# Kernel optimization log

Measured on AMD Instinct MI355X. Metric: run time of the kernel, lower is better.

## Reference

```python
import jax, jax.numpy as jnp
import numpy as np

N_STEPS = 2
MAX_STEP = 1.0
EPS64 = float(np.finfo(np.float64).eps)


def _sphere_log(p, q):
    # log map on unit sphere, tangent at p pointing to q; p,q: [..., D]
    cos = jnp.clip(jnp.sum(p * q, axis=-1, keepdims=True), -1.0, 1.0)
    u = q - cos * p
    un = jnp.linalg.norm(u, axis=-1, keepdims=True)
    theta = jnp.arccos(cos)
    return theta * u / (un + 1e-12)


def _sphere_exp(p, v):
    # exp map on unit sphere; jnp.sinc(n/pi) = sin(n)/n (stable at 0)
    n = jnp.linalg.norm(v, axis=-1, keepdims=True)
    x = jnp.cos(n) * p + jnp.sinc(n / jnp.pi) * v
    return x / jnp.linalg.norm(x, axis=-1, keepdims=True)


def setup_inputs() -> dict:
    key = jax.random.key(0)
    ks = jax.random.split(key, 6)
    N, C, D, E = 50000, 16, 3, 1600000
    nodes = jax.random.normal(ks[0], (N, C, D), dtype=jnp.float32)
    nodes = nodes / jnp.linalg.norm(nodes, axis=-1, keepdims=True)  # points on S^2
    edge_w = jax.random.uniform(ks[1], (E,), dtype=jnp.float32)
    senders = jax.random.randint(ks[2], (E,), 0, N, dtype=jnp.int32)
    receivers = jax.random.randint(ks[3], (E,), 0, N, dtype=jnp.int32)
    t_sqrt = 1.0 + 0.3 * jax.random.normal(ks[4], (C,), dtype=jnp.float32)
    delta_sqrt = 1.0 + 0.3 * jax.random.normal(ks[5], (C,), dtype=jnp.float32)
    return {"nodes": nodes, "edge_w": edge_w, "t_sqrt": t_sqrt,
            "delta_sqrt": delta_sqrt, "senders": senders, "receivers": receivers}


def reference(nodes, edge_w, t_sqrt, delta_sqrt, senders, receivers):
    N = nodes.shape[0]
    t = (t_sqrt ** 2) / N_STEPS            # per-channel time, split across Euler steps
    delta = delta_sqrt ** 2                 # per-channel min step size
    deg = jax.ops.segment_sum(edge_w, senders, num_segments=N)  # [N]

    def laplace(x):
        # graph Laplacian of manifold-valued signal: weighted mean of log maps, negated
        logs = _sphere_log(x[senders], x[receivers])              # [E, C, D]
        agg = jax.ops.segment_sum(edge_w[:, None, None] * logs, senders, num_segments=N)
        return -agg / (deg[:, None, None] + 1e-12)                # [N, C, D]

    def step(x, _):
        v = laplace(x)
        nrm = jnp.sqrt(jnp.sum(v * v, axis=-1) + EPS64)           # [N, C]
        alp = jax.nn.sigmoid(nrm - delta[None, :])
        scale = jnp.where(nrm * alp <= MAX_STEP, alp, MAX_STEP / nrm)
        v = -(v * scale[..., None]) * t[None, :, None]
        return _sphere_exp(x, v), None

    x, _ = jax.lax.scan(step, nodes, None, length=N_STEPS, unroll=N_STEPS)
    return x
```

## Files before the change

kernel.cpp:

```cpp
#include <hip/hip_runtime.h>
#include <math.h>


constexpr float EPS64F = 2.2204460492503131e-16f;
constexpr float PI_F   = 3.14159265358979323846f;
constexpr int   NREP   = 8;

typedef int   vi4 __attribute__((ext_vector_type(4)));
typedef float vf4 __attribute__((ext_vector_type(4)));
typedef float vf2 __attribute__((ext_vector_type(2)));


__global__ __launch_bounds__(256) void hist_kernel(
    const vi4* __restrict__ snd4, int* __restrict__ rep,
    vi4* __restrict__ pos4, const int* __restrict__ snd,
    int* __restrict__ pos, int N, int E) {
  int tid = threadIdx.x;
  int E4 = E >> 2;
  #pragma unroll
  for (int gg = 0; gg < 4; ++gg) {
    int g = blockIdx.x * 1024 + gg * 256 + tid;
    if (g < E4) {
      int rb = (g & (NREP - 1)) * N;
      vi4 s = __builtin_nontemporal_load(&snd4[g]);
      vi4 p;
      p.x = atomicAdd(&rep[rb + s.x], 1);
      p.y = atomicAdd(&rep[rb + s.y], 1);
      p.z = atomicAdd(&rep[rb + s.z], 1);
      p.w = atomicAdd(&rep[rb + s.w], 1);
      __builtin_nontemporal_store(p, &pos4[g]);
    }
  }
  if (blockIdx.x == 0 && tid == 0) {
    for (int e = E4 << 2; e < E; ++e) pos[e] = atomicAdd(&rep[snd[e]], 1);
  }
}

__global__ __launch_bounds__(1024) void scanA_kernel(
    int* __restrict__ rep, int* __restrict__ row_start,
    int* __restrict__ btot, int N) {
  __shared__ int wsum[16];
  int tid = threadIdx.x;
  int lane = tid & 63, wave = tid >> 6;
  int i = blockIdx.x * 1024 + tid;
  int v = 0;
  if (i < N) {
    int run = 0;
    int cpre[NREP];
    #pragma unroll
    for (int r = 0; r < NREP; ++r) {
      int t = rep[r * N + i];
      cpre[r] = run;
      run += t;
    }
    v = run;
    #pragma unroll
    for (int r = 0; r < NREP; ++r) rep[r * N + i] = cpre[r];
  }
  int incl = v;
  #pragma unroll
  for (int off = 1; off < 64; off <<= 1) {
    int t = __shfl_up(incl, off, 64);
    if (lane >= off) incl += t;
  }
  if (lane == 63) wsum[wave] = incl;
  __syncthreads();
  if (wave == 0 && lane < 16) {
    int wincl = wsum[lane];
    #pragma unroll
    for (int off = 1; off < 16; off <<= 1) {
      int t = __shfl_up(wincl, off, 64);
      if (lane >= off) wincl += t;
    }
    wsum[lane] = wincl;
  }
  __syncthreads();
  int woff = (wave > 0) ? wsum[wave - 1] : 0;
  if (i < N) row_start[i] = woff + incl - v;
  if (tid == 0) btot[blockIdx.x] = wsum[15];
}

__global__ __launch_bounds__(64) void scanB_kernel(
    const int* __restrict__ btot, int* __restrict__ boff,
    int* __restrict__ row_start, int nb, int N) {
  int lane = threadIdx.x;
  int v = (lane < nb) ? btot[lane] : 0;
  int incl = v;
  #pragma unroll
  for (int off = 1; off < 64; off <<= 1) {
    int t = __shfl_up(incl, off, 64);
    if (lane >= off) incl += t;
  }
  if (lane < nb) boff[lane] = incl - v;
  if (lane == 63) row_start[N] = incl;
}

__global__ __launch_bounds__(1024) void scanC_kernel(
    int* __restrict__ row_start, const int* __restrict__ boff,
    int* __restrict__ rep, int N) {
  int i = blockIdx.x * 1024 + threadIdx.x;
  if (i < N) {
    int rs = row_start[i] + boff[blockIdx.x];
    row_start[i] = rs;
    #pragma unroll
    for (int r = 0; r < NREP; ++r) rep[r * N + i] += rs;
  }
}

__global__ __launch_bounds__(256) void fill_kernel(
    const vi4* __restrict__ snd4, const vi4* __restrict__ rcv4,
    const vf4* __restrict__ ew4, const vi4* __restrict__ pos4,
    const int* __restrict__ rep, long long* __restrict__ pair,
    const int* __restrict__ snd, const int* __restrict__ rcv,
    const float* __restrict__ ew, const int* __restrict__ pos, int N, int E) {
  int tid = threadIdx.x;
  int E4 = E >> 2;
  #pragma unroll
  for (int gg = 0; gg < 2; ++gg) {
    int g = blockIdx.x * 512 + gg * 256 + tid;
    if (g < E4) {
      int rb = (g & (NREP - 1)) * N;
      vi4 s = __builtin_nontemporal_load(&snd4[g]);
      vi4 r = __builtin_nontemporal_load(&rcv4[g]);
      vf4 w = __builtin_nontemporal_load(&ew4[g]);
      vi4 p = __builtin_nontemporal_load(&pos4[g]);
      pair[rep[rb + s.x] + p.x] =
          (long long)(((unsigned long long)(unsigned)__float_as_int(w.x) << 32) | (unsigned)(r.x * 48));
      pair[rep[rb + s.y] + p.y] =
          (long long)(((unsigned long long)(unsigned)__float_as_int(w.y) << 32) | (unsigned)(r.y * 48));
      pair[rep[rb + s.z] + p.z] =
          (long long)(((unsigned long long)(unsigned)__float_as_int(w.z) << 32) | (unsigned)(r.z * 48));
      pair[rep[rb + s.w] + p.w] =
          (long long)(((unsigned long long)(unsigned)__float_as_int(w.w) << 32) | (unsigned)(r.w * 48));
    }
  }
  if (blockIdx.x == 0 && tid == 0) {
    for (int e = E4 << 2; e < E; ++e) {
      pair[rep[snd[e]] + pos[e]] =
          (long long)(((unsigned long long)(unsigned)__float_as_int(ew[e]) << 32) | (unsigned)(rcv[e] * 48));
    }
    for (int z = 0; z < 16; ++z) pair[(size_t)E + z] = 0;
  }
}


__device__ __forceinline__ void edge_accum_pk(
    vf2 p0, vf2 p1, vf2 p2, vf2 q0, vf2 q1, vf2 q2, vf2 w,
    vf2& a0, vf2& a1, vf2& a2) {
  vf2 cs = p0 * q0 + p1 * q1 + p2 * q2;
  cs = __builtin_elementwise_min(vf2{1.f, 1.f},
       __builtin_elementwise_max(vf2{-1.f, -1.f}, cs));
  vf2 u0 = q0 - cs * p0;
  vf2 u1 = q1 - cs * p1;
  vf2 u2 = q2 - cs * p2;
  vf2 un2 = __builtin_elementwise_max(u0 * u0 + u1 * u1 + u2 * u2,
                                      vf2{1e-24f, 1e-24f});
  vf2 ax = __builtin_elementwise_abs(cs);
  vf2 s = __builtin_elementwise_sqrt(vf2{1.f, 1.f} - ax);
  vf2 poly = ((ax * -0.0187293f + 0.0742610f) * ax - 0.2121144f) * ax
             + 1.5707288f;
  vf2 th = s * poly;
  vf2 theta;
  theta.x = (cs.x >= 0.0f) ? th.x : (PI_F - th.x);
  theta.y = (cs.y >= 0.0f) ? th.y : (PI_F - th.y);
  vf2 rsq;
  rsq.x = __builtin_amdgcn_rsqf(un2.x);
  rsq.y = __builtin_amdgcn_rsqf(un2.y);
  vf2 coef = w * theta * rsq;
  a0 += coef * u0;
  a1 += coef * u1;
  a2 += coef * u2;
}

__device__ __forceinline__ void node_step(
    float a0, float a1, float a2, float ws, float p0, float p1, float p2,
    float ts, float dsv, float& y0, float& y1, float& y2) {
  float invdg = __builtin_amdgcn_rcpf(ws + 1e-12f);
  float g0 = a0 * invdg, g1 = a1 * invdg, g2 = a2 * invdg;
  float nrm = sqrtf(fmaf(g0, g0, fmaf(g1, g1, g2 * g2)) + EPS64F);
  float tch = ts * ts * 0.5f;
  float dch = dsv * dsv;
  float alp = __builtin_amdgcn_rcpf(1.0f + __expf(dch - nrm));
  float scale = (nrm * alp <= 1.0f) ? alp : __builtin_amdgcn_rcpf(nrm);
  float f = scale * tch;
  float v0 = g0 * f, v1 = g1 * f, v2 = g2 * f;
  float nv = sqrtf(fmaf(v0, v0, fmaf(v1, v1, v2 * v2)));
  float cn = __cosf(nv);
  float sc = (nv > 1e-20f) ? (__sinf(nv) * __builtin_amdgcn_rcpf(nv)) : 1.0f;
  float t0 = fmaf(cn, p0, sc * v0);
  float t1 = fmaf(cn, p1, sc * v1);
  float t2 = fmaf(cn, p2, sc * v2);
  float inv = __builtin_amdgcn_rsqf(fmaf(t0, t0, fmaf(t1, t1, t2 * t2)));
  y0 = t0 * inv; y1 = t1 * inv; y2 = t2 * inv;
}

__global__ __launch_bounds__(256) void flowp_kernel(
    const float* __restrict__ xin, const int* __restrict__ row_start,
    const long long* __restrict__ pair, const float* __restrict__ tsq,
    const float* __restrict__ dsq, float* __restrict__ xout, int N) {
  int node = blockIdx.x * 4 + (threadIdx.x >> 6);
  if (node >= N) return;
  int lane = threadIdx.x & 63;
  int c = lane & 15;
  int k = lane >> 4;
  int c3 = c * 3;
  int beg = row_start[node];
  int end = row_start[node + 1];
  int ip = node * 48 + c3;
  float ps0 = xin[ip], ps1 = xin[ip + 1], ps2 = xin[ip + 2];
  vf2 p0 = {ps0, ps0}, p1 = {ps1, ps1}, p2 = {ps2, ps2};
  vf2 a0 = {0.f, 0.f}, a1 = {0.f, 0.f}, a2 = {0.f, 0.f}, wsv = {0.f, 0.f};
  int iters = (end - beg + 15) >> 4;
  int j = beg + k;
  for (int t = 0; t < iters; ++t, j += 16) {
    long long e0 = __builtin_nontemporal_load(&pair[j]);
    long long e1 = __builtin_nontemporal_load(&pair[j + 4]);
    long long e2 = __builtin_nontemporal_load(&pair[j + 8]);
    long long e3 = __builtin_nontemporal_load(&pair[j + 12]);
    float w0 = (j      < end) ? __int_as_float((int)(e0 >> 32)) : 0.f;
    float w1 = (j + 4  < end) ? __int_as_float((int)(e1 >> 32)) : 0.f;
    float w2 = (j + 8  < end) ? __int_as_float((int)(e2 >> 32)) : 0.f;
    float w3 = (j + 12 < end) ? __int_as_float((int)(e3 >> 32)) : 0.f;
    const float* q0p = xin + ((int)e0 + c3);
    const float* q1p = xin + ((int)e1 + c3);
    const float* q2p = xin + ((int)e2 + c3);
    const float* q3p = xin + ((int)e3 + c3);
    float qa0 = q0p[0], qa1 = q0p[1], qa2 = q0p[2];
    float qb0 = q1p[0], qb1 = q1p[1], qb2 = q1p[2];
    float qc0 = q2p[0], qc1 = q2p[1], qc2 = q2p[2];
    float qd0 = q3p[0], qd1 = q3p[1], qd2 = q3p[2];
    vf2 wA = {w0, w1}, wB = {w2, w3};
    edge_accum_pk(p0, p1, p2, vf2{qa0, qb0}, vf2{qa1, qb1}, vf2{qa2, qb2},
                  wA, a0, a1, a2);
    edge_accum_pk(p0, p1, p2, vf2{qc0, qd0}, vf2{qc1, qd1}, vf2{qc2, qd2},
                  wB, a0, a1, a2);
    wsv += wA + wB;
  }
  float A0 = a0.x + a0.y, A1 = a1.x + a1.y, A2 = a2.x + a2.y;
  float ws = wsv.x + wsv.y;
  A0 += __shfl_xor(A0, 16); A1 += __shfl_xor(A1, 16);
  A2 += __shfl_xor(A2, 16); ws += __shfl_xor(ws, 16);
  A0 += __shfl_xor(A0, 32); A1 += __shfl_xor(A1, 32);
  A2 += __shfl_xor(A2, 32); ws += __shfl_xor(ws, 32);
  if (k == 0) {
    float y0, y1, y2;
    node_step(A0, A1, A2, ws, ps0, ps1, ps2, tsq[c], dsq[c], y0, y1, y2);
    xout[ip] = y0; xout[ip + 1] = y1; xout[ip + 2] = y2;
  }
}

static inline size_t al16(size_t x) { return (x + 15) & ~(size_t)15; }

extern "C" void kernel_launch(void* const* d_in, const int* in_sizes, int n_in,
                              void* d_out, int out_size, void* d_ws, size_t ws_size,
                              hipStream_t stream) {
  const float* nodes = (const float*)d_in[0];
  const float* ew    = (const float*)d_in[1];
  const float* tsq   = (const float*)d_in[2];
  const float* dsq   = (const float*)d_in[3];
  const int*   snd   = (const int*)d_in[4];
  const int*   rcv   = (const int*)d_in[5];
  float* out = (float*)d_out;

  int E = in_sizes[1];
  int N = in_sizes[0] / 48;

  size_t repB  = al16((size_t)NREP * N * 4);
  size_t rsB   = al16((size_t)(N + 4) * 4);
  size_t auxB  = 512;
  size_t pairB = al16((size_t)(E + 16) * 8);

  char* base = (char*)d_ws;
  int*       rep       = (int*)base;
  int*       row_start = (int*)(base + repB);
  int*       btot      = (int*)(base + repB + rsB);
  int*       boff      = btot + 64;
  long long* pair      = (long long*)(base + repB + rsB + auxB);
  char*      after     = base + repB + rsB + auxB + pairB;
  int*       pos       = (int*)after;
  float*     xtmp      = (float*)after;

  hipMemsetAsync(rep, 0, repB, stream);

  int E4 = E >> 2;
  int hb  = (E4 + 1023) / 1024;
  int fbk = (E4 + 511) / 512;
  int nb  = (N + 1023) / 1024;
  int nfb = (N + 3) / 4;

  hist_kernel<<<hb, 256, 0, stream>>>((const vi4*)snd, rep, (vi4*)pos,
                                      snd, pos, N, E);
  scanA_kernel<<<nb, 1024, 0, stream>>>(rep, row_start, btot, N);
  scanB_kernel<<<1, 64, 0, stream>>>(btot, boff, row_start, nb, N);
  scanC_kernel<<<nb, 1024, 0, stream>>>(row_start, boff, rep, N);
  fill_kernel<<<fbk, 256, 0, stream>>>((const vi4*)snd, (const vi4*)rcv,
                                       (const vf4*)ew, (const vi4*)pos,
                                       rep, pair, snd, rcv, ew, pos, N, E);

  flowp_kernel<<<nfb, 256, 0, stream>>>(nodes, row_start, pair, tsq, dsq, xtmp, N);
  flowp_kernel<<<nfb, 256, 0, stream>>>(xtmp, row_start, pair, tsq, dsq, out, N);
}
```

Baseline: 309.1 us.

## Pad node coordinates to float4 for single vector gathers in flow kernels

Converts the node array from packed xyz (12 bytes per channel) to a padded float4 layout, so each neighbor gather in the edge loop becomes one 16-byte load instead of three scalar loads. The pair index now encodes receiver*16 in float4 units, and the intermediate state between the two steps is kept padded. A fallback path handles small workspaces by gathering from the original layout in the first step. This adds a conversion kernel and a third more gathered bytes per node, and sets a launch-bounds occupancy hint.

Measured after the change: 340.7 us. 1.1x slower.

```diff
diff --git a/kernel.cpp b/kernel.cpp
--- a/kernel.cpp
+++ b/kernel.cpp
@@ -125,22 +125,32 @@
       vf4 w = __builtin_nontemporal_load(&ew4[g]);
       vi4 p = __builtin_nontemporal_load(&pos4[g]);
       pair[rep[rb + s.x] + p.x] =
-          (long long)(((unsigned long long)(unsigned)__float_as_int(w.x) << 32) | (unsigned)(r.x * 48));
+          (long long)(((unsigned long long)(unsigned)__float_as_int(w.x) << 32) | (unsigned)(r.x * 16));
       pair[rep[rb + s.y] + p.y] =
-          (long long)(((unsigned long long)(unsigned)__float_as_int(w.y) << 32) | (unsigned)(r.y * 48));
+          (long long)(((unsigned long long)(unsigned)__float_as_int(w.y) << 32) | (unsigned)(r.y * 16));
       pair[rep[rb + s.z] + p.z] =
-          (long long)(((unsigned long long)(unsigned)__float_as_int(w.z) << 32) | (unsigned)(r.z * 48));
+          (long long)(((unsigned long long)(unsigned)__float_as_int(w.z) << 32) | (unsigned)(r.z * 16));
       pair[rep[rb + s.w] + p.w] =
-          (long long)(((unsigned long long)(unsigned)__float_as_int(w.w) << 32) | (unsigned)(r.w * 48));
+          (long long)(((unsigned long long)(unsigned)__float_as_int(w.w) << 32) | (unsigned)(r.w * 16));
     }
   }
   if (blockIdx.x == 0 && tid == 0) {
     for (int e = E4 << 2; e < E; ++e) {
       pair[rep[snd[e]] + pos[e]] =
-          (long long)(((unsigned long long)(unsigned)__float_as_int(ew[e]) << 32) | (unsigned)(rcv[e] * 48));
+          (long long)(((unsigned long long)(unsigned)__float_as_int(ew[e]) << 32) | (unsigned)(rcv[e] * 16));
     }
     for (int z = 0; z < 16; ++z) pair[(size_t)E + z] = 0;
   }
+}
+
+
+__global__ __launch_bounds__(256) void conv_kernel(
+    const float* __restrict__ xf, vf4* __restrict__ xp, int NC) {
+  int t = blockIdx.x * 256 + threadIdx.x;
+  if (t >= NC) return;
+  vf4 v;
+  v.x = xf[t * 3]; v.y = xf[t * 3 + 1]; v.z = xf[t * 3 + 2]; v.w = 0.f;
+  xp[t] = v;
 }
 
 
@@ -194,10 +204,66 @@
   y0 = t0 * inv; y1 = t1 * inv; y2 = t2 * inv;
 }
 
-__global__ __launch_bounds__(256) void flowp_kernel(
-    const float* __restrict__ xin, const int* __restrict__ row_start,
+__global__ __launch_bounds__(256, 8) void flow4_kernel(
+    const vf4* __restrict__ xp, const int* __restrict__ row_start,
     const long long* __restrict__ pair, const float* __restrict__ tsq,
-    const float* __restrict__ dsq, float* __restrict__ xout, int N) {
+    const float* __restrict__ dsq, vf4* __restrict__ yp,
+    float* __restrict__ out48, int N) {
+  int node = blockIdx.x * 4 + (threadIdx.x >> 6);
+  if (node >= N) return;
+  int lane = threadIdx.x & 63;
+  int c = lane & 15;
+  int k = lane >> 4;
+  int beg = row_start[node];
+  int end = row_start[node + 1];
+  vf4 p = xp[node * 16 + c];
+  vf2 p0 = {p.x, p.x}, p1 = {p.y, p.y}, p2 = {p.z, p.z};
+  vf2 a0 = {0.f, 0.f}, a1 = {0.f, 0.f}, a2 = {0.f, 0.f}, wsv = {0.f, 0.f};
+  int iters = (end - beg + 15) >> 4;
+  int j = beg + k;
+  for (int t = 0; t < iters; ++t, j += 16) {
+    long long e0 = __builtin_nontemporal_load(&pair[j]);
+    long long e1 = __builtin_nontemporal_load(&pair[j + 4]);
+    long long e2 = __builtin_nontemporal_load(&pair[j + 8]);
+    long long e3 = __builtin_nontemporal_load(&pair[j + 12]);
+    float w0 = (j      < end) ? __int_as_float((int)(e0 >> 32)) : 0.f;
+    float w1 = (j + 4  < end) ? __int_as_float((int)(e1 >> 32)) : 0.f;
+    float w2 = (j + 8  < end) ? __int_as_float((int)(e2 >> 32)) : 0.f;
+    float w3 = (j + 12 < end) ? __int_as_float((int)(e3 >> 32)) : 0.f;
+    vf4 qa = xp[(int)e0 + c];
+    vf4 qb = xp[(int)e1 + c];
+    vf4 qc = xp[(int)e2 + c];
+    vf4 qd = xp[(int)e3 + c];
+    vf2 wA = {w0, w1}, wB = {w2, w3};
+    edge_accum_pk(p0, p1, p2, vf2{qa.x, qb.x}, vf2{qa.y, qb.y},
+                  vf2{qa.z, qb.z}, wA, a0, a1, a2);
+    edge_accum_pk(p0, p1, p2, vf2{qc.x, qd.x}, vf2{qc.y, qd.y},
+                  vf2{qc.z, qd.z}, wB, a0, a1, a2);
+    wsv += wA + wB;
+  }
+  float A0 = a0.x + a0.y, A1 = a1.x + a1.y, A2 = a2.x + a2.y;
+  float ws = wsv.x + wsv.y;
+  A0 += __shfl_xor(A0, 16); A1 += __shfl_xor(A1, 16);
+  A2 += __shfl_xor(A2, 16); ws += __shfl_xor(ws, 16);
+  A0 += __shfl_xor(A0, 32); A1 += __shfl_xor(A1, 32);
+  A2 += __shfl_xor(A2, 32); ws += __shfl_xor(ws, 32);
+  if (k == 0) {
+    float y0, y1, y2;
+    node_step(A0, A1, A2, ws, p.x, p.y, p.z, tsq[c], dsq[c], y0, y1, y2);
+    if (out48) {
+      int ip = node * 48 + c * 3;
+      out48[ip] = y0; out48[ip + 1] = y1; out48[ip + 2] = y2;
+    } else {
+      vf4 v; v.x = y0; v.y = y1; v.z = y2; v.w = 0.f;
+      yp[node * 16 + c] = v;
+    }
+  }
+}
+
+__global__ __launch_bounds__(256) void flow3_kernel(
+    const float* __restrict__ x48, const int* __restrict__ row_start,
+    const long long* __restrict__ pair, const float* __restrict__ tsq,
+    const float* __restrict__ dsq, vf4* __restrict__ yp, int N) {
   int node = blockIdx.x * 4 + (threadIdx.x >> 6);
   if (node >= N) return;
   int lane = threadIdx.x & 63;
@@ -207,7 +273,7 @@
   int beg = row_start[node];
   int end = row_start[node + 1];
   int ip = node * 48 + c3;
-  float ps0 = xin[ip], ps1 = xin[ip + 1], ps2 = xin[ip + 2];
+  float ps0 = x48[ip], ps1 = x48[ip + 1], ps2 = x48[ip + 2];
   vf2 p0 = {ps0, ps0}, p1 = {ps1, ps1}, p2 = {ps2, ps2};
   vf2 a0 = {0.f, 0.f}, a1 = {0.f, 0.f}, a2 = {0.f, 0.f}, wsv = {0.f, 0.f};
   int iters = (end - beg + 15) >> 4;
@@ -221,10 +287,10 @@
     float w1 = (j + 4  < end) ? __int_as_float((int)(e1 >> 32)) : 0.f;
     float w2 = (j + 8  < end) ? __int_as_float((int)(e2 >> 32)) : 0.f;
     float w3 = (j + 12 < end) ? __int_as_float((int)(e3 >> 32)) : 0.f;
-    const float* q0p = xin + ((int)e0 + c3);
-    const float* q1p = xin + ((int)e1 + c3);
-    const float* q2p = xin + ((int)e2 + c3);
-    const float* q3p = xin + ((int)e3 + c3);
+    const float* q0p = x48 + ((int)e0 * 3 + c3);
+    const float* q1p = x48 + ((int)e1 * 3 + c3);
+    const float* q2p = x48 + ((int)e2 * 3 + c3);
+    const float* q3p = x48 + ((int)e3 * 3 + c3);
     float qa0 = q0p[0], qa1 = q0p[1], qa2 = q0p[2];
     float qb0 = q1p[0], qb1 = q1p[1], qb2 = q1p[2];
     float qc0 = q2p[0], qc1 = q2p[1], qc2 = q2p[2];
@@ -245,7 +311,8 @@
   if (k == 0) {
     float y0, y1, y2;
     node_step(A0, A1, A2, ws, ps0, ps1, ps2, tsq[c], dsq[c], y0, y1, y2);
-    xout[ip] = y0; xout[ip + 1] = y1; xout[ip + 2] = y2;
+    vf4 v; v.x = y0; v.y = y1; v.z = y2; v.w = 0.f;
+    yp[node * 16 + c] = v;
   }
 }
 
@@ -269,6 +336,10 @@
   size_t rsB   = al16((size_t)(N + 4) * 4);
   size_t auxB  = 512;
   size_t pairB = al16((size_t)(E + 16) * 8);
+  size_t xpB   = al16((size_t)N * 16 * 16);
+  size_t posB  = al16((size_t)E * 4);
+  size_t zB    = (posB > xpB) ? posB : xpB;
+  size_t need_main = repB + rsB + auxB + pairB + xpB + zB;
 
   char* base = (char*)d_ws;
   int*       rep       = (int*)base;
@@ -277,8 +348,12 @@
   int*       boff      = btot + 64;
   long long* pair      = (long long*)(base + repB + rsB + auxB);
   char*      after     = base + repB + rsB + auxB + pairB;
-  int*       pos       = (int*)after;
-  float*     xtmp      = (float*)after;
+
+  bool mainp = (ws_size >= need_main);
+  vf4* xpA = (vf4*)after;
+  char* zreg = mainp ? (after + xpB) : after;
+  int* pos = (int*)zreg;
+  vf4* xpB_ = (vf4*)zreg;
 
   hipMemsetAsync(rep, 0, repB, stream);
 
@@ -286,8 +361,10 @@
   int hb  = (E4 + 1023) / 1024;
   int fbk = (E4 + 511) / 512;
   int nb  = (N + 1023) / 1024;
+  int cb  = (N * 16 + 255) / 256;
   int nfb = (N + 3) / 4;
 
+  if (mainp) conv_kernel<<<cb, 256, 0, stream>>>(nodes, xpA, N * 16);
   hist_kernel<<<hb, 256, 0, stream>>>((const vi4*)snd, rep, (vi4*)pos,
                                       snd, pos, N, E);
   scanA_kernel<<<nb, 1024, 0, stream>>>(rep, row_start, btot, N);
@@ -297,6 +374,15 @@
                                        (const vf4*)ew, (const vi4*)pos,
                                        rep, pair, snd, rcv, ew, pos, N, E);
 
-  flowp_kernel<<<nfb, 256, 0, stream>>>(nodes, row_start, pair, tsq, dsq, xtmp, N);
-  flowp_kernel<<<nfb, 256, 0, stream>>>(xtmp, row_start, pair, tsq, dsq, out, N);
-}
+  if (mainp) {
+    flow4_kernel<<<nfb, 256, 0, stream>>>(xpA, row_start, pair, tsq, dsq,
+                                          xpB_, (float*)0, N);
+    flow4_kernel<<<nfb, 256, 0, stream>>>(xpB_, row_start, pair, tsq, dsq,
+                                          (vf4*)0, out, N);
+  } else {
+    flow3_kernel<<<nfb, 256, 0, stream>>>(nodes, row_start, pair, tsq, dsq,
+                                          xpB_, N);
+    flow4_kernel<<<nfb, 256, 0, stream>>>(xpB_, row_start, pair, tsq, dsq,
+                                          (vf4*)0, out, N);
+  }
+}
```

## Replace global-atomic sender histogram with chunked LDS histograms and byte offsets

Applied to the files above, without the earlier changes.

Builds the CSR for the edge list with per-chunk shared-memory histograms instead of global atomics on replicated counters. Edges are split into 32K-edge chunks and sender ranges of 16K nodes, and the within-bucket positions are stored as bytes. A per-chunk scan then produces base offsets for the fill kernel. This removes global atomic contention and the memset, and shrinks the position array. In exchange every chunk block rereads the sender array once per sender range, there are extra scan passes over a chunk-by-N offset table, and the byte positions assume fewer than 256 edges per sender in each chunk.

Result: faster. 298.4 us (-3.4%).

```diff
diff --git a/kernel.cpp b/kernel.cpp
--- a/kernel.cpp
+++ b/kernel.cpp
@@ -4,59 +4,71 @@
 
 constexpr float EPS64F = 2.2204460492503131e-16f;
 constexpr float PI_F   = 3.14159265358979323846f;
-constexpr int   NREP   = 8;
+constexpr int   SR_BITS = 14;
+constexpr int   CH_BITS = 15;
 
 typedef int   vi4 __attribute__((ext_vector_type(4)));
 typedef float vf4 __attribute__((ext_vector_type(4)));
 typedef float vf2 __attribute__((ext_vector_type(2)));
 
 
-__global__ __launch_bounds__(256) void hist_kernel(
-    const vi4* __restrict__ snd4, int* __restrict__ rep,
-    vi4* __restrict__ pos4, const int* __restrict__ snd,
-    int* __restrict__ pos, int N, int E) {
+__global__ __launch_bounds__(256) void lhist_kernel(
+    const int* __restrict__ snd, unsigned char* __restrict__ pos,
+    int* __restrict__ partial2, int E, int NC) {
+  __shared__ int h[1 << SR_BITS];
   int tid = threadIdx.x;
-  int E4 = E >> 2;
-  #pragma unroll
-  for (int gg = 0; gg < 4; ++gg) {
-    int g = blockIdx.x * 1024 + gg * 256 + tid;
-    if (g < E4) {
-      int rb = (g & (NREP - 1)) * N;
-      vi4 s = __builtin_nontemporal_load(&snd4[g]);
-      vi4 p;
-      p.x = atomicAdd(&rep[rb + s.x], 1);
-      p.y = atomicAdd(&rep[rb + s.y], 1);
-      p.z = atomicAdd(&rep[rb + s.z], 1);
-      p.w = atomicAdd(&rep[rb + s.w], 1);
-      __builtin_nontemporal_store(p, &pos4[g]);
+  int c = blockIdx.x, s = blockIdx.y;
+  for (int i = tid; i < (1 << SR_BITS); i += 256) h[i] = 0;
+  __syncthreads();
+  int base = c << CH_BITS;
+  int cnt = min(1 << CH_BITS, E - base);
+  int s0 = s << SR_BITS;
+  const vi4* snd4 = (const vi4*)(snd + base);
+  int cnt4 = cnt >> 2;
+  for (int i = tid; i < cnt4; i += 256) {
+    vi4 sv = snd4[i];
+    int e = base + (i << 2);
+    int v;
+    v = sv.x - s0; if ((unsigned)v < (1u << SR_BITS)) pos[e]     = (unsigned char)atomicAdd(&h[v], 1);
+    v = sv.y - s0; if ((unsigned)v < (1u << SR_BITS)) pos[e + 1] = (unsigned char)atomicAdd(&h[v], 1);
+    v = sv.z - s0; if ((unsigned)v < (1u << SR_BITS)) pos[e + 2] = (unsigned char)atomicAdd(&h[v], 1);
+    v = sv.w - s0; if ((unsigned)v < (1u << SR_BITS)) pos[e + 3] = (unsigned char)atomicAdd(&h[v], 1);
+  }
+  if (tid == 0) {
+    for (int i = cnt4 << 2; i < cnt; ++i) {
+      int v = snd[base + i] - s0;
+      if ((unsigned)v < (1u << SR_BITS))
+        pos[base + i] = (unsigned char)atomicAdd(&h[v], 1);
     }
   }
-  if (blockIdx.x == 0 && tid == 0) {
-    for (int e = E4 << 2; e < E; ++e) pos[e] = atomicAdd(&rep[snd[e]], 1);
-  }
+  __syncthreads();
+  int* dst = partial2 + ((size_t)(s * NC + c) << SR_BITS);
+  for (int i = tid; i < (1 << SR_BITS); i += 256) dst[i] = h[i];
+}
+
+__global__ __launch_bounds__(256) void scan1_kernel(
+    const int* __restrict__ partial2, int* __restrict__ boff,
+    int* __restrict__ tot, int N, int NC) {
+  int v = blockIdx.x * 256 + threadIdx.x;
+  if (v >= N) return;
+  int s = v >> SR_BITS, lv = v & ((1 << SR_BITS) - 1);
+  int run = 0;
+  for (int c = 0; c < NC; ++c) {
+    int t = partial2[((size_t)(s * NC + c) << SR_BITS) + lv];
+    boff[(size_t)c * N + v] = run;
+    run += t;
+  }
+  tot[v] = run;
 }
 
 __global__ __launch_bounds__(1024) void scanA_kernel(
-    int* __restrict__ rep, int* __restrict__ row_start,
+    const int* __restrict__ tot, int* __restrict__ row_start,
     int* __restrict__ btot, int N) {
   __shared__ int wsum[16];
   int tid = threadIdx.x;
   int lane = tid & 63, wave = tid >> 6;
   int i = blockIdx.x * 1024 + tid;
-  int v = 0;
-  if (i < N) {
-    int run = 0;
-    int cpre[NREP];
-    #pragma unroll
-    for (int r = 0; r < NREP; ++r) {
-      int t = rep[r * N + i];
-      cpre[r] = run;
-      run += t;
-    }
-    v = run;
-    #pragma unroll
-    for (int r = 0; r < NREP; ++r) rep[r * N + i] = cpre[r];
-  }
+  int v = (i < N) ? tot[i] : 0;
   int incl = v;
   #pragma unroll
   for (int off = 1; off < 64; off <<= 1) {
@@ -81,7 +93,7 @@
 }
 
 __global__ __launch_bounds__(64) void scanB_kernel(
-    const int* __restrict__ btot, int* __restrict__ boff,
+    const int* __restrict__ btot, int* __restrict__ boffb,
     int* __restrict__ row_start, int nb, int N) {
   int lane = threadIdx.x;
   int v = (lane < nb) ? btot[lane] : 0;
@@ -91,52 +103,55 @@
     int t = __shfl_up(incl, off, 64);
     if (lane >= off) incl += t;
   }
-  if (lane < nb) boff[lane] = incl - v;
+  if (lane < nb) boffb[lane] = incl - v;
   if (lane == 63) row_start[N] = incl;
 }
 
 __global__ __launch_bounds__(1024) void scanC_kernel(
-    int* __restrict__ row_start, const int* __restrict__ boff,
-    int* __restrict__ rep, int N) {
+    int* __restrict__ row_start, const int* __restrict__ boffb, int N) {
   int i = blockIdx.x * 1024 + threadIdx.x;
-  if (i < N) {
-    int rs = row_start[i] + boff[blockIdx.x];
-    row_start[i] = rs;
-    #pragma unroll
-    for (int r = 0; r < NREP; ++r) rep[r * N + i] += rs;
-  }
+  if (i < N) row_start[i] += boffb[blockIdx.x];
+}
+
+__global__ __launch_bounds__(256) void scanD_kernel(
+    int* __restrict__ boff, const int* __restrict__ row_start, int N, int NC) {
+  int v = blockIdx.x * 256 + threadIdx.x;
+  if (v >= N) return;
+  int rs = row_start[v];
+  for (int c = 0; c < NC; ++c) boff[(size_t)c * N + v] += rs;
 }
 
 __global__ __launch_bounds__(256) void fill_kernel(
     const vi4* __restrict__ snd4, const vi4* __restrict__ rcv4,
-    const vf4* __restrict__ ew4, const vi4* __restrict__ pos4,
-    const int* __restrict__ rep, long long* __restrict__ pair,
+    const vf4* __restrict__ ew4, const unsigned char* __restrict__ pos,
+    const int* __restrict__ boff, long long* __restrict__ pair,
     const int* __restrict__ snd, const int* __restrict__ rcv,
-    const float* __restrict__ ew, const int* __restrict__ pos, int N, int E) {
+    const float* __restrict__ ew, int N, int E) {
   int tid = threadIdx.x;
   int E4 = E >> 2;
   #pragma unroll
   for (int gg = 0; gg < 2; ++gg) {
     int g = blockIdx.x * 512 + gg * 256 + tid;
     if (g < E4) {
-      int rb = (g & (NREP - 1)) * N;
+      int e = g << 2;
+      const int* bc = boff + (size_t)(e >> CH_BITS) * N;
       vi4 s = __builtin_nontemporal_load(&snd4[g]);
       vi4 r = __builtin_nontemporal_load(&rcv4[g]);
       vf4 w = __builtin_nontemporal_load(&ew4[g]);
-      vi4 p = __builtin_nontemporal_load(&pos4[g]);
-      pair[rep[rb + s.x] + p.x] =
+      unsigned pb = *(const unsigned*)(pos + e);
+      pair[bc[s.x] + (pb & 255u)] =
           (long long)(((unsigned long long)(unsigned)__float_as_int(w.x) << 32) | (unsigned)(r.x * 48));
-      pair[rep[rb + s.y] + p.y] =
+      pair[bc[s.y] + ((pb >> 8) & 255u)] =
           (long long)(((unsigned long long)(unsigned)__float_as_int(w.y) << 32) | (unsigned)(r.y * 48));
-      pair[rep[rb + s.z] + p.z] =
+      pair[bc[s.z] + ((pb >> 16) & 255u)] =
           (long long)(((unsigned long long)(unsigned)__float_as_int(w.z) << 32) | (unsigned)(r.z * 48));
-      pair[rep[rb + s.w] + p.w] =
+      pair[bc[s.w] + (pb >> 24)] =
           (long long)(((unsigned long long)(unsigned)__float_as_int(w.w) << 32) | (unsigned)(r.w * 48));
     }
   }
   if (blockIdx.x == 0 && tid == 0) {
     for (int e = E4 << 2; e < E; ++e) {
-      pair[rep[snd[e]] + pos[e]] =
+      pair[boff[(size_t)(e >> CH_BITS) * N + snd[e]] + pos[e]] =
           (long long)(((unsigned long long)(unsigned)__float_as_int(ew[e]) << 32) | (unsigned)(rcv[e] * 48));
     }
     for (int z = 0; z < 16; ++z) pair[(size_t)E + z] = 0;
@@ -265,37 +280,42 @@
   int E = in_sizes[1];
   int N = in_sizes[0] / 48;
 
-  size_t repB  = al16((size_t)NREP * N * 4);
+  int NS = (N + (1 << SR_BITS) - 1) >> SR_BITS;
+  int NC = (E + (1 << CH_BITS) - 1) >> CH_BITS;
+
   size_t rsB   = al16((size_t)(N + 4) * 4);
   size_t auxB  = 512;
   size_t pairB = al16((size_t)(E + 16) * 8);
+  size_t p2B   = al16(((size_t)NS * NC << SR_BITS) * 4);
+  size_t boffB = al16((size_t)NC * N * 4);
+  size_t totB  = al16((size_t)N * 4);
 
   char* base = (char*)d_ws;
-  int*       rep       = (int*)base;
-  int*       row_start = (int*)(base + repB);
-  int*       btot      = (int*)(base + repB + rsB);
-  int*       boff      = btot + 64;
-  long long* pair      = (long long*)(base + repB + rsB + auxB);
-  char*      after     = base + repB + rsB + auxB + pairB;
-  int*       pos       = (int*)after;
-  float*     xtmp      = (float*)after;
-
-  hipMemsetAsync(rep, 0, repB, stream);
-
-  int E4 = E >> 2;
-  int hb  = (E4 + 1023) / 1024;
+  int*           row_start = (int*)base;
+  int*           btot      = (int*)(base + rsB);
+  int*           boffb     = btot + 64;
+  long long*     pair      = (long long*)(base + rsB + auxB);
+  int*           partial2  = (int*)(base + rsB + auxB + pairB);
+  int*           boff      = (int*)(base + rsB + auxB + pairB + p2B);
+  int*           tot       = (int*)(base + rsB + auxB + pairB + p2B + boffB);
+  unsigned char* pos       = (unsigned char*)(base + rsB + auxB + pairB + p2B + boffB + totB);
+  float*         xtmp      = (float*)partial2;
+
+  int E4  = E >> 2;
+  int nb  = (N + 1023) / 1024;
+  int nb2 = (N + 255) / 256;
   int fbk = (E4 + 511) / 512;
-  int nb  = (N + 1023) / 1024;
   int nfb = (N + 3) / 4;
 
-  hist_kernel<<<hb, 256, 0, stream>>>((const vi4*)snd, rep, (vi4*)pos,
-                                      snd, pos, N, E);
-  scanA_kernel<<<nb, 1024, 0, stream>>>(rep, row_start, btot, N);
-  scanB_kernel<<<1, 64, 0, stream>>>(btot, boff, row_start, nb, N);
-  scanC_kernel<<<nb, 1024, 0, stream>>>(row_start, boff, rep, N);
+  lhist_kernel<<<dim3(NC, NS), 256, 0, stream>>>(snd, pos, partial2, E, NC);
+  scan1_kernel<<<nb2, 256, 0, stream>>>(partial2, boff, tot, N, NC);
+  scanA_kernel<<<nb, 1024, 0, stream>>>(tot, row_start, btot, N);
+  scanB_kernel<<<1, 64, 0, stream>>>(btot, boffb, row_start, nb, N);
+  scanC_kernel<<<nb, 1024, 0, stream>>>(row_start, boffb, N);
+  scanD_kernel<<<nb2, 256, 0, stream>>>(boff, row_start, N, NC);
   fill_kernel<<<fbk, 256, 0, stream>>>((const vi4*)snd, (const vi4*)rcv,
-                                       (const vf4*)ew, (const vi4*)pos,
-                                       rep, pair, snd, rcv, ew, pos, N, E);
+                                       (const vf4*)ew, pos, boff, pair,
+                                       snd, rcv, ew, N, E);
 
   flowp_kernel<<<nfb, 256, 0, stream>>>(nodes, row_start, pair, tsq, dsq, xtmp, N);
   flowp_kernel<<<nfb, 256, 0, stream>>>(xtmp, row_start, pair, tsq, dsq, out, N);
```
